# Performance work log

Hardware: AMD Instinct MI355X
Metric: run time of the kernel (lower is better)

Reference implementation:

```python
import jax, jax.numpy as jnp
import numpy as np

NUM_HEADS = 16
HEAD_DIM = 64
Q_DIM = K_DIM = V_DIM = 1024
LQ = LK = 4096
TAU = HEAD_DIM ** (-0.5)


def setup_inputs() -> dict:
    key = jax.random.key(0)
    ks = jax.random.split(key, 11)
    inner = NUM_HEADS * HEAD_DIM
    s = 0.02
    return {
        "q": jax.random.normal(ks[0], (LQ, Q_DIM), dtype=jnp.float32),
        "k": jax.random.normal(ks[1], (LK, K_DIM), dtype=jnp.float32),
        "v": jax.random.normal(ks[2], (LK, V_DIM), dtype=jnp.float32),
        "Wq": jax.random.normal(ks[3], (Q_DIM, inner), dtype=jnp.float32) * s,
        "bq": jax.random.normal(ks[4], (inner,), dtype=jnp.float32) * s,
        "Wk": jax.random.normal(ks[5], (K_DIM, inner), dtype=jnp.float32) * s,
        "bk": jax.random.normal(ks[6], (inner,), dtype=jnp.float32) * s,
        "Wv": jax.random.normal(ks[7], (V_DIM, inner), dtype=jnp.float32) * s,
        "bv": jax.random.normal(ks[8], (inner,), dtype=jnp.float32) * s,
        "Wo": jax.random.normal(ks[9], (inner, Q_DIM), dtype=jnp.float32) * s,
        "bo": jax.random.normal(ks[10], (Q_DIM,), dtype=jnp.float32) * s,
    }


def reference(q, k, v, Wq, bq, Wk, bk, Wv, bv, Wo, bo):
    h, x = NUM_HEADS, HEAD_DIM
    # projections: [L, h*x] -> per-head layout
    qh = (q @ Wq + bq).reshape(-1, h, x)  # [Lq, h, x]
    kh = (k @ Wk + bk).reshape(-1, h, x)  # [Lk, h, x]
    vh = (v @ Wv + bv).reshape(-1, h, x)  # [Lk, h, x]
    # scores: [h, Lq, Lk]
    att = jnp.einsum('qhx,khx->hqk', qh, kh) * TAU
    att = jax.nn.softmax(att, axis=-1)  # dropout=0.0 -> identity
    ctx = jnp.einsum('hqk,khx->qhx', att, vh).reshape(-1, h * x)  # [Lq, h*x]
    out = ctx @ Wo + bo  # [Lq, Q_DIM]
    return out, att
```

## Files before the change

kernel.cpp:

```cpp
#include <hip/hip_runtime.h>
#include <hip/hip_bf16.h>

typedef unsigned short ushort_t;
typedef __attribute__((ext_vector_type(8))) short short8;
typedef __attribute__((ext_vector_type(8))) __bf16 bf16x8;
typedef __attribute__((ext_vector_type(4))) float f32x4;

#define LQS 4096
#define LKS 4096
#define NH 16
#define HD 64
#define DIN 1024
static constexpr float TAU_S = 0.125f;

__device__ __forceinline__ ushort_t f32_to_bf16(float x) {
  union { float f; unsigned u; } v; v.f = x;
  unsigned r = v.u + 0x7FFF + ((v.u >> 16) & 1);
  return (ushort_t)(r >> 16);
}

__device__ __forceinline__ void gld_lds16(const void* g, void* l) {
  __builtin_amdgcn_global_load_lds((const __attribute__((address_space(1))) void*)g,
                                   (__attribute__((address_space(3))) void*)l, 16, 0, 0);
}

__device__ __forceinline__ f32x4 mfma16(bf16x8 a, bf16x8 b, f32x4 c) {
  return __builtin_amdgcn_mfma_f32_16x16x32_bf16(a, b, c, 0, 0, 0);
}

__global__ void cvt_kernel(const float* __restrict__ src, ushort_t* __restrict__ dst, int n) {
  int i = (blockIdx.x * 256 + threadIdx.x) * 8;
  if (i + 8 > n) return;
  float4 a = *(const float4*)(src + i);
  float4 b = *(const float4*)(src + i + 4);
  short8 o;
  o[0] = (short)f32_to_bf16(a.x); o[1] = (short)f32_to_bf16(a.y);
  o[2] = (short)f32_to_bf16(a.z); o[3] = (short)f32_to_bf16(a.w);
  o[4] = (short)f32_to_bf16(b.x); o[5] = (short)f32_to_bf16(b.y);
  o[6] = (short)f32_to_bf16(b.z); o[7] = (short)f32_to_bf16(b.w);
  *(short8*)(dst + i) = o;
}

__global__ void transpose_w(const float* __restrict__ W, ushort_t* __restrict__ Wt) {
  __shared__ float tile[64][65];
  const int t = threadIdx.x;
  const int k0 = blockIdx.y * 64, n0 = blockIdx.x * 64;
#pragma unroll
  for (int i = 0; i < 16; ++i) {
    int idx = i * 256 + t;
    int r = idx >> 6, c = idx & 63;
    tile[r][c] = W[(size_t)(k0 + r) * DIN + n0 + c];
  }
  __syncthreads();
#pragma unroll
  for (int i = 0; i < 16; ++i) {
    int idx = i * 256 + t;
    int r = idx >> 6, c = idx & 63;
    Wt[(size_t)(n0 + r) * DIN + k0 + c] = f32_to_bf16(tile[c][r]);
  }
}

__global__ void transpose_v(const ushort_t* __restrict__ vh, ushort_t* __restrict__ vt) {
  __shared__ ushort_t tile[64][65];
  const int t = threadIdx.x;
  const int k0 = blockIdx.x * 64, h = blockIdx.y;
#pragma unroll
  for (int i = 0; i < 16; ++i) {
    int idx = i * 256 + t;
    int r = idx >> 6, c = idx & 63;
    tile[r][c] = vh[(size_t)(k0 + r) * DIN + h * HD + c];
  }
  __syncthreads();
#pragma unroll
  for (int i = 0; i < 16; ++i) {
    int idx = i * 256 + t;
    int r = idx >> 6, c = idx & 63;
    vt[((size_t)h * HD + r) * (size_t)LKS + k0 + c] = tile[c][r];
  }
}

template <bool OUT_F32>
__launch_bounds__(256, 2)
__global__ void gemm_nt(const ushort_t* __restrict__ A, const ushort_t* __restrict__ Bt,
                        const float* __restrict__ bias, void* __restrict__ Cout,
                        int M, int N, int K, float scale) {
  __shared__ __align__(16) ushort_t Alds[128 * 64];
  __shared__ __align__(16) ushort_t Blds[128 * 64];
  const int t = threadIdx.x, wave = t >> 6, lane = t & 63;
  const int l15 = lane & 15, lg = lane >> 4;
  const int m0 = blockIdx.y * 128, n0 = blockIdx.x * 128;
  const int wr = wave >> 1, wc = wave & 1;
  f32x4 acc[4][4];
#pragma unroll
  for (int i = 0; i < 4; ++i)
#pragma unroll
    for (int j = 0; j < 4; ++j) acc[i][j] = (f32x4){0.f, 0.f, 0.f, 0.f};

  for (int tk = 0; tk < K / 64; ++tk) {
#pragma unroll
    for (int c = 0; c < 4; ++c) {
      int chunk = wave * 4 + c;
      int row = chunk * 8 + (lane >> 3);
      int ss = (lane & 7) ^ (row & 7);
      gld_lds16(A + (size_t)(m0 + row) * K + tk * 64 + ss * 8, (char*)Alds + chunk * 1024);
      gld_lds16(Bt + (size_t)(n0 + row) * K + tk * 64 + ss * 8, (char*)Blds + chunk * 1024);
    }
    __syncthreads();
#pragma unroll
    for (int kk = 0; kk < 2; ++kk) {
      bf16x8 a[4], b[4];
#pragma unroll
      for (int i = 0; i < 4; ++i) {
        int ra = wr * 64 + i * 16 + l15;
        a[i] = *(const bf16x8*)((const char*)Alds + ra * 128 + ((((kk * 4 + lg) << 4)) ^ ((ra & 7) << 4)));
        int rb = wc * 64 + i * 16 + l15;
        b[i] = *(const bf16x8*)((const char*)Blds + rb * 128 + ((((kk * 4 + lg) << 4)) ^ ((rb & 7) << 4)));
      }
#pragma unroll
      for (int mi = 0; mi < 4; ++mi)
#pragma unroll
        for (int ni = 0; ni < 4; ++ni)
          acc[mi][ni] = mfma16(a[mi], b[ni], acc[mi][ni]);
    }
    __syncthreads();
  }
#pragma unroll
  for (int ni = 0; ni < 4; ++ni) {
    int coln = n0 + wc * 64 + ni * 16 + l15;
    float bv = bias[coln];
#pragma unroll
    for (int mi = 0; mi < 4; ++mi) {
#pragma unroll
      for (int r = 0; r < 4; ++r) {
        int rowm = m0 + wr * 64 + mi * 16 + lg * 4 + r;
        float v = (acc[mi][ni][r] + bv) * scale;
        if (OUT_F32)
          ((float*)Cout)[(size_t)rowm * N + coln] = v;
        else
          ((ushort_t*)Cout)[(size_t)rowm * N + coln] = f32_to_bf16(v);
      }
    }
  }
}

__launch_bounds__(256, 2)
__global__ void attn_kernel(const ushort_t* __restrict__ qh, const ushort_t* __restrict__ kh,
                            const ushort_t* __restrict__ vt, float* __restrict__ att,
                            ushort_t* __restrict__ ctx) {
  __shared__ __align__(16) ushort_t Klds[64 * 64];
  __shared__ __align__(16) ushort_t Vlds[64 * 64];
  __shared__ __align__(16) ushort_t Plds[64 * 64];
  const int t = threadIdx.x, wave = t >> 6, lane = t & 63;
  const int l15 = lane & 15, lg = lane >> 4;
  const int h = blockIdx.y;
  const int q0 = blockIdx.x * 64;

  bf16x8 qa[2];
  {
    int row = q0 + wave * 16 + l15;
    const ushort_t* qp = qh + (size_t)row * DIN + h * HD + lg * 8;
    qa[0] = *(const bf16x8*)(qp);
    qa[1] = *(const bf16x8*)(qp + 32);
  }

  float rs[4] = {0.f, 0.f, 0.f, 0.f};
  for (int tk = 0; tk < LKS / 64; ++tk) {
#pragma unroll
    for (int c = 0; c < 2; ++c) {
      int chunk = wave * 2 + c;
      int row = chunk * 8 + (lane >> 3);
      int ss = (lane & 7) ^ (row & 7);
      gld_lds16(kh + (size_t)(tk * 64 + row) * DIN + h * HD + ss * 8, (char*)Klds + chunk * 1024);
    }
    __syncthreads();
#pragma unroll
    for (int ct = 0; ct < 4; ++ct) {
      f32x4 acc = (f32x4){0.f, 0.f, 0.f, 0.f};
#pragma unroll
      for (int kk = 0; kk < 2; ++kk) {
        int row = ct * 16 + l15;
        bf16x8 kb = *(const bf16x8*)((const char*)Klds + row * 128 + ((((kk * 4 + lg) << 4)) ^ ((row & 7) << 4)));
        acc = mfma16(qa[kk], kb, acc);
      }
#pragma unroll
      for (int r = 0; r < 4; ++r) rs[r] += __expf(acc[r]);
    }
    __syncthreads();
  }
#pragma unroll
  for (int m = 1; m < 16; m <<= 1) {
#pragma unroll
    for (int r = 0; r < 4; ++r) rs[r] += __shfl_xor(rs[r], m, 64);
  }
  float recip[4];
#pragma unroll
  for (int r = 0; r < 4; ++r) recip[r] = 1.0f / rs[r];

  f32x4 cacc[4];
#pragma unroll
  for (int x = 0; x < 4; ++x) cacc[x] = (f32x4){0.f, 0.f, 0.f, 0.f};
  float* atth = att + ((size_t)h << 24);

  for (int tk = 0; tk < LKS / 64; ++tk) {
#pragma unroll
    for (int c = 0; c < 2; ++c) {
      int chunk = wave * 2 + c;
      int row = chunk * 8 + (lane >> 3);
      int ss = (lane & 7) ^ (row & 7);
      gld_lds16(kh + (size_t)(tk * 64 + row) * DIN + h * HD + ss * 8, (char*)Klds + chunk * 1024);
      gld_lds16(vt + ((size_t)h * HD + row) * (size_t)LKS + tk * 64 + ss * 8, (char*)Vlds + chunk * 1024);
    }
    __syncthreads();
#pragma unroll
    for (int ct = 0; ct < 4; ++ct) {
      f32x4 acc = (f32x4){0.f, 0.f, 0.f, 0.f};
#pragma unroll
      for (int kk = 0; kk < 2; ++kk) {
        int row = ct * 16 + l15;
        bf16x8 kb = *(const bf16x8*)((const char*)Klds + row * 128 + ((((kk * 4 + lg) << 4)) ^ ((row & 7) << 4)));
        acc = mfma16(qa[kk], kb, acc);
      }
#pragma unroll
      for (int r = 0; r < 4; ++r) {
        float p = __expf(acc[r]) * recip[r];
        int rowq = q0 + wave * 16 + lg * 4 + r;
        int col = tk * 64 + ct * 16 + l15;
        atth[((size_t)rowq << 12) + col] = p;
        int R = wave * 16 + lg * 4 + r;
        int byte = R * 128 + ((ct * 32 + l15 * 2) ^ ((R & 7) << 4));
        *(ushort_t*)((char*)Plds + byte) = f32_to_bf16(p);
      }
    }
    bf16x8 pa[2];
#pragma unroll
    for (int kk = 0; kk < 2; ++kk) {
      int R = wave * 16 + l15;
      pa[kk] = *(const bf16x8*)((const char*)Plds + R * 128 + ((((kk * 4 + lg) << 4)) ^ ((R & 7) << 4)));
    }
#pragma unroll
    for (int x = 0; x < 4; ++x) {
#pragma unroll
      for (int kk = 0; kk < 2; ++kk) {
        int rv = x * 16 + l15;
        bf16x8 vb = *(const bf16x8*)((const char*)Vlds + rv * 128 + ((((kk * 4 + lg) << 4)) ^ ((rv & 7) << 4)));
        cacc[x] = mfma16(pa[kk], vb, cacc[x]);
      }
    }
    __syncthreads();
  }
#pragma unroll
  for (int x = 0; x < 4; ++x) {
#pragma unroll
    for (int r = 0; r < 4; ++r) {
      int rowq = q0 + wave * 16 + lg * 4 + r;
      int col = h * HD + x * 16 + l15;
      ctx[(size_t)rowq * DIN + col] = f32_to_bf16(cacc[x][r]);
    }
  }
}

extern "C" void kernel_launch(void* const* d_in, const int* in_sizes, int n_in,
                              void* d_out, int out_size, void* d_ws, size_t ws_size,
                              hipStream_t stream) {
  const float* q = (const float*)d_in[0];
  const float* k = (const float*)d_in[1];
  const float* v = (const float*)d_in[2];
  const float* Wq = (const float*)d_in[3];
  const float* bq = (const float*)d_in[4];
  const float* Wk = (const float*)d_in[5];
  const float* bk = (const float*)d_in[6];
  const float* Wv = (const float*)d_in[7];
  const float* bv = (const float*)d_in[8];
  const float* Wo = (const float*)d_in[9];
  const float* bo = (const float*)d_in[10];

  float* out = (float*)d_out;
  float* att = out + (size_t)LQS * DIN;

  char* ws = (char*)d_ws;
  ushort_t* qhb = (ushort_t*)(ws + (size_t)0);
  ushort_t* khb = (ushort_t*)(ws + ((size_t)8 << 20));
  ushort_t* vhb = (ushort_t*)(ws + ((size_t)16 << 20));
  ushort_t* vtb = (ushort_t*)(ws + ((size_t)24 << 20));
  ushort_t* ctx = (ushort_t*)(ws + ((size_t)32 << 20));
  ushort_t* qb = (ushort_t*)(ws + ((size_t)40 << 20));
  ushort_t* kb = (ushort_t*)(ws + ((size_t)48 << 20));
  ushort_t* vb = (ushort_t*)(ws + ((size_t)56 << 20));
  ushort_t* Wqt = (ushort_t*)(ws + ((size_t)64 << 20));
  ushort_t* Wkt = (ushort_t*)(ws + ((size_t)66 << 20));
  ushort_t* Wvt = (ushort_t*)(ws + ((size_t)68 << 20));
  ushort_t* Wot = (ushort_t*)(ws + ((size_t)70 << 20));

  const int n = LQS * DIN;
  cvt_kernel<<<n / 8 / 256, 256, 0, stream>>>(q, qb, n);
  cvt_kernel<<<n / 8 / 256, 256, 0, stream>>>(k, kb, n);
  cvt_kernel<<<n / 8 / 256, 256, 0, stream>>>(v, vb, n);

  dim3 tg(16, 16);
  transpose_w<<<tg, 256, 0, stream>>>(Wq, Wqt);
  transpose_w<<<tg, 256, 0, stream>>>(Wk, Wkt);
  transpose_w<<<tg, 256, 0, stream>>>(Wv, Wvt);
  transpose_w<<<tg, 256, 0, stream>>>(Wo, Wot);

  dim3 gg(DIN / 128, LQS / 128);
  gemm_nt<false><<<gg, 256, 0, stream>>>(qb, Wqt, bq, qhb, LQS, DIN, DIN, TAU_S);
  gemm_nt<false><<<gg, 256, 0, stream>>>(kb, Wkt, bk, khb, LQS, DIN, DIN, 1.0f);
  gemm_nt<false><<<gg, 256, 0, stream>>>(vb, Wvt, bv, vhb, LQS, DIN, DIN, 1.0f);

  transpose_v<<<dim3(64, 16), 256, 0, stream>>>(vhb, vtb);

  attn_kernel<<<dim3(LQS / 64, NH), 256, 0, stream>>>(qhb, khb, vtb, att, ctx);

  gemm_nt<true><<<gg, 256, 0, stream>>>(ctx, Wot, bo, out, LQS, DIN, DIN, 1.0f);
}
```

Before: 472.6 us.

## Double-buffer K/V tiles in attention, batch launches, and use exp2 with folded scale

The attention kernel now runs 512-thread blocks over 128 query rows. K and V tiles are double-buffered in LDS so the next tile's load overlaps the current tile's compute, and each wave keeps a private P buffer. Softmax switches from __expf to hardware exp2, with log2(e) folded into the Q projection scale. The three conversion kernels, four weight transposes and three projection GEMMs are each merged into one batched launch via blockIdx.z, cutting launch count. The larger block and extra LDS may reduce occupancy; the output is still dominated by writing the full fp32 attention matrix.

```diff
diff --git a/kernel.cpp b/kernel.cpp
--- a/kernel.cpp
+++ b/kernel.cpp
@@ -11,7 +11,12 @@
 #define NH 16
 #define HD 64
 #define DIN 1024
+#define QBLK 128
+#define KVB 64
 static constexpr float TAU_S = 0.125f;
+static constexpr float LOG2E = 1.4426950408889634f;
+
+__device__ __forceinline__ float exp2_fast(float x) { return __builtin_amdgcn_exp2f(x); }
 
 __device__ __forceinline__ ushort_t f32_to_bf16(float x) {
   union { float f; unsigned u; } v; v.f = x;
@@ -28,9 +33,11 @@
   return __builtin_amdgcn_mfma_f32_16x16x32_bf16(a, b, c, 0, 0, 0);
 }
 
-__global__ void cvt_kernel(const float* __restrict__ src, ushort_t* __restrict__ dst, int n) {
+struct Cvt3 { const float* src[3]; ushort_t* dst[3]; };
+__global__ void cvt_kernel(Cvt3 c) {
+  const float* __restrict__ src = c.src[blockIdx.y];
+  ushort_t* __restrict__ dst = c.dst[blockIdx.y];
   int i = (blockIdx.x * 256 + threadIdx.x) * 8;
-  if (i + 8 > n) return;
   float4 a = *(const float4*)(src + i);
   float4 b = *(const float4*)(src + i + 4);
   short8 o;
@@ -41,7 +48,10 @@
   *(short8*)(dst + i) = o;
 }
 
-__global__ void transpose_w(const float* __restrict__ W, ushort_t* __restrict__ Wt) {
+struct TW4 { const float* W[4]; ushort_t* Wt[4]; };
+__global__ void transpose_w(TW4 w) {
+  const float* __restrict__ W = w.W[blockIdx.z];
+  ushort_t* __restrict__ Wt = w.Wt[blockIdx.z];
   __shared__ float tile[64][65];
   const int t = threadIdx.x;
   const int k0 = blockIdx.y * 64, n0 = blockIdx.x * 64;
@@ -79,11 +89,24 @@
   }
 }
 
+struct Batch3 {
+  const ushort_t* A[3];
+  const ushort_t* Bt[3];
+  const float* bias[3];
+  void* C[3];
+  float scale[3];
+};
 template <bool OUT_F32>
 __launch_bounds__(256, 2)
-__global__ void gemm_nt(const ushort_t* __restrict__ A, const ushort_t* __restrict__ Bt,
-                        const float* __restrict__ bias, void* __restrict__ Cout,
-                        int M, int N, int K, float scale) {
+__global__ void gemm_nt(Batch3 bt3) {
+  const int z = blockIdx.z;
+  const ushort_t* __restrict__ A = bt3.A[z];
+  const ushort_t* __restrict__ Bt = bt3.Bt[z];
+  const float* __restrict__ bias = bt3.bias[z];
+  void* __restrict__ Cout = bt3.C[z];
+  const float scale = bt3.scale[z];
+  const int K = DIN, N = DIN;
+
   __shared__ __align__(16) ushort_t Alds[128 * 64];
   __shared__ __align__(16) ushort_t Blds[128 * 64];
   const int t = threadIdx.x, wave = t >> 6, lane = t & 63;
@@ -143,17 +166,22 @@
   }
 }
 
-__launch_bounds__(256, 2)
+__launch_bounds__(512, 4)
 __global__ void attn_kernel(const ushort_t* __restrict__ qh, const ushort_t* __restrict__ kh,
                             const ushort_t* __restrict__ vt, float* __restrict__ att,
                             ushort_t* __restrict__ ctx) {
-  __shared__ __align__(16) ushort_t Klds[64 * 64];
-  __shared__ __align__(16) ushort_t Vlds[64 * 64];
-  __shared__ __align__(16) ushort_t Plds[64 * 64];
+  __shared__ __align__(16) ushort_t Klds[2][KVB * 64];
+  __shared__ __align__(16) ushort_t Vlds[2][KVB * 64];
+  __shared__ __align__(16) ushort_t Plds[8][16 * KVB];
   const int t = threadIdx.x, wave = t >> 6, lane = t & 63;
   const int l15 = lane & 15, lg = lane >> 4;
   const int h = blockIdx.y;
-  const int q0 = blockIdx.x * 64;
+  const int q0 = blockIdx.x * QBLK;
+
+  const int srow = t >> 3;
+  const int sslot = (t & 7) ^ (srow & 7);
+  const ushort_t* kbase = kh + (size_t)srow * DIN + h * HD + sslot * 8;
+  const ushort_t* vbase = vt + ((size_t)h * HD + srow) * (size_t)LKS + sslot * 8;
 
   bf16x8 qa[2];
   {
@@ -164,28 +192,26 @@
   }
 
   float rs[4] = {0.f, 0.f, 0.f, 0.f};
-  for (int tk = 0; tk < LKS / 64; ++tk) {
-#pragma unroll
-    for (int c = 0; c < 2; ++c) {
-      int chunk = wave * 2 + c;
-      int row = chunk * 8 + (lane >> 3);
-      int ss = (lane & 7) ^ (row & 7);
-      gld_lds16(kh + (size_t)(tk * 64 + row) * DIN + h * HD + ss * 8, (char*)Klds + chunk * 1024);
-    }
-    __syncthreads();
+  gld_lds16(kbase, (char*)Klds[0] + wave * 1024);
+  __syncthreads();
+  int cur = 0;
+  for (int tk = 0; tk < LKS / KVB; ++tk) {
+    if (tk + 1 < LKS / KVB)
+      gld_lds16(kbase + (size_t)(tk + 1) * KVB * DIN, (char*)Klds[cur ^ 1] + wave * 1024);
 #pragma unroll
     for (int ct = 0; ct < 4; ++ct) {
       f32x4 acc = (f32x4){0.f, 0.f, 0.f, 0.f};
 #pragma unroll
       for (int kk = 0; kk < 2; ++kk) {
         int row = ct * 16 + l15;
-        bf16x8 kb = *(const bf16x8*)((const char*)Klds + row * 128 + ((((kk * 4 + lg) << 4)) ^ ((row & 7) << 4)));
+        bf16x8 kb = *(const bf16x8*)((const char*)Klds[cur] + row * 128 + ((((kk * 4 + lg) << 4)) ^ ((row & 7) << 4)));
         acc = mfma16(qa[kk], kb, acc);
       }
 #pragma unroll
-      for (int r = 0; r < 4; ++r) rs[r] += __expf(acc[r]);
+      for (int r = 0; r < 4; ++r) rs[r] += exp2_fast(acc[r]);
     }
     __syncthreads();
+    cur ^= 1;
   }
 #pragma unroll
   for (int m = 1; m < 16; m <<= 1) {
@@ -201,52 +227,52 @@
   for (int x = 0; x < 4; ++x) cacc[x] = (f32x4){0.f, 0.f, 0.f, 0.f};
   float* atth = att + ((size_t)h << 24);
 
-  for (int tk = 0; tk < LKS / 64; ++tk) {
-#pragma unroll
-    for (int c = 0; c < 2; ++c) {
-      int chunk = wave * 2 + c;
-      int row = chunk * 8 + (lane >> 3);
-      int ss = (lane & 7) ^ (row & 7);
-      gld_lds16(kh + (size_t)(tk * 64 + row) * DIN + h * HD + ss * 8, (char*)Klds + chunk * 1024);
-      gld_lds16(vt + ((size_t)h * HD + row) * (size_t)LKS + tk * 64 + ss * 8, (char*)Vlds + chunk * 1024);
-    }
-    __syncthreads();
+  gld_lds16(kbase, (char*)Klds[0] + wave * 1024);
+  gld_lds16(vbase, (char*)Vlds[0] + wave * 1024);
+  __syncthreads();
+  cur = 0;
+  for (int tk = 0; tk < LKS / KVB; ++tk) {
+    if (tk + 1 < LKS / KVB) {
+      gld_lds16(kbase + (size_t)(tk + 1) * KVB * DIN, (char*)Klds[cur ^ 1] + wave * 1024);
+      gld_lds16(vbase + (tk + 1) * KVB, (char*)Vlds[cur ^ 1] + wave * 1024);
+    }
 #pragma unroll
     for (int ct = 0; ct < 4; ++ct) {
       f32x4 acc = (f32x4){0.f, 0.f, 0.f, 0.f};
 #pragma unroll
       for (int kk = 0; kk < 2; ++kk) {
         int row = ct * 16 + l15;
-        bf16x8 kb = *(const bf16x8*)((const char*)Klds + row * 128 + ((((kk * 4 + lg) << 4)) ^ ((row & 7) << 4)));
+        bf16x8 kb = *(const bf16x8*)((const char*)Klds[cur] + row * 128 + ((((kk * 4 + lg) << 4)) ^ ((row & 7) << 4)));
         acc = mfma16(qa[kk], kb, acc);
       }
 #pragma unroll
       for (int r = 0; r < 4; ++r) {
-        float p = __expf(acc[r]) * recip[r];
+        float p = exp2_fast(acc[r]) * recip[r];
         int rowq = q0 + wave * 16 + lg * 4 + r;
-        int col = tk * 64 + ct * 16 + l15;
+        int col = tk * KVB + ct * 16 + l15;
         atth[((size_t)rowq << 12) + col] = p;
-        int R = wave * 16 + lg * 4 + r;
+        int R = lg * 4 + r;
         int byte = R * 128 + ((ct * 32 + l15 * 2) ^ ((R & 7) << 4));
-        *(ushort_t*)((char*)Plds + byte) = f32_to_bf16(p);
+        *(ushort_t*)((char*)Plds[wave] + byte) = f32_to_bf16(p);
       }
     }
     bf16x8 pa[2];
 #pragma unroll
     for (int kk = 0; kk < 2; ++kk) {
-      int R = wave * 16 + l15;
-      pa[kk] = *(const bf16x8*)((const char*)Plds + R * 128 + ((((kk * 4 + lg) << 4)) ^ ((R & 7) << 4)));
+      int R = l15;
+      pa[kk] = *(const bf16x8*)((const char*)Plds[wave] + R * 128 + ((((kk * 4 + lg) << 4)) ^ ((R & 7) << 4)));
     }
 #pragma unroll
     for (int x = 0; x < 4; ++x) {
 #pragma unroll
       for (int kk = 0; kk < 2; ++kk) {
         int rv = x * 16 + l15;
-        bf16x8 vb = *(const bf16x8*)((const char*)Vlds + rv * 128 + ((((kk * 4 + lg) << 4)) ^ ((rv & 7) << 4)));
+        bf16x8 vb = *(const bf16x8*)((const char*)Vlds[cur] + rv * 128 + ((((kk * 4 + lg) << 4)) ^ ((rv & 7) << 4)));
         cacc[x] = mfma16(pa[kk], vb, cacc[x]);
       }
     }
     __syncthreads();
+    cur ^= 1;
   }
 #pragma unroll
   for (int x = 0; x < 4; ++x) {
@@ -291,25 +317,33 @@
   ushort_t* Wvt = (ushort_t*)(ws + ((size_t)68 << 20));
   ushort_t* Wot = (ushort_t*)(ws + ((size_t)70 << 20));
 
-  const int n = LQS * DIN;
-  cvt_kernel<<<n / 8 / 256, 256, 0, stream>>>(q, qb, n);
-  cvt_kernel<<<n / 8 / 256, 256, 0, stream>>>(k, kb, n);
-  cvt_kernel<<<n / 8 / 256, 256, 0, stream>>>(v, vb, n);
-
-  dim3 tg(16, 16);
-  transpose_w<<<tg, 256, 0, stream>>>(Wq, Wqt);
-  transpose_w<<<tg, 256, 0, stream>>>(Wk, Wkt);
-  transpose_w<<<tg, 256, 0, stream>>>(Wv, Wvt);
-  transpose_w<<<tg, 256, 0, stream>>>(Wo, Wot);
-
-  dim3 gg(DIN / 128, LQS / 128);
-  gemm_nt<false><<<gg, 256, 0, stream>>>(qb, Wqt, bq, qhb, LQS, DIN, DIN, TAU_S);
-  gemm_nt<false><<<gg, 256, 0, stream>>>(kb, Wkt, bk, khb, LQS, DIN, DIN, 1.0f);
-  gemm_nt<false><<<gg, 256, 0, stream>>>(vb, Wvt, bv, vhb, LQS, DIN, DIN, 1.0f);
+  Cvt3 c3;
+  c3.src[0] = q; c3.src[1] = k; c3.src[2] = v;
+  c3.dst[0] = qb; c3.dst[1] = kb; c3.dst[2] = vb;
+  cvt_kernel<<<dim3(LQS * DIN / 8 / 256, 3), 256, 0, stream>>>(c3);
+
+  TW4 w4;
+  w4.W[0] = Wq; w4.W[1] = Wk; w4.W[2] = Wv; w4.W[3] = Wo;
+  w4.Wt[0] = Wqt; w4.Wt[1] = Wkt; w4.Wt[2] = Wvt; w4.Wt[3] = Wot;
+  transpose_w<<<dim3(16, 16, 4), 256, 0, stream>>>(w4);
+
+  Batch3 pb;
+  pb.A[0] = qb; pb.A[1] = kb; pb.A[2] = vb;
+  pb.Bt[0] = Wqt; pb.Bt[1] = Wkt; pb.Bt[2] = Wvt;
+  pb.bias[0] = bq; pb.bias[1] = bk; pb.bias[2] = bv;
+  pb.C[0] = qhb; pb.C[1] = khb; pb.C[2] = vhb;
+  pb.scale[0] = TAU_S * LOG2E; pb.scale[1] = 1.0f; pb.scale[2] = 1.0f;
+  gemm_nt<false><<<dim3(DIN / 128, LQS / 128, 3), 256, 0, stream>>>(pb);
 
   transpose_v<<<dim3(64, 16), 256, 0, stream>>>(vhb, vtb);
 
-  attn_kernel<<<dim3(LQS / 64, NH), 256, 0, stream>>>(qhb, khb, vtb, att, ctx);
-
-  gemm_nt<true><<<gg, 256, 0, stream>>>(ctx, Wot, bo, out, LQS, DIN, DIN, 1.0f);
-}
+  attn_kernel<<<dim3(LQS / QBLK, NH), 512, 0, stream>>>(qhb, khb, vtb, att, ctx);
+
+  Batch3 ob;
+  ob.A[0] = ctx; ob.A[1] = ctx; ob.A[2] = ctx;
+  ob.Bt[0] = Wot; ob.Bt[1] = Wot; ob.Bt[2] = Wot;
+  ob.bias[0] = bo; ob.bias[1] = bo; ob.bias[2] = bo;
+  ob.C[0] = out; ob.C[1] = out; ob.C[2] = out;
+  ob.scale[0] = 1.0f; ob.scale[1] = 1.0f; ob.scale[2] = 1.0f;
+  gemm_nt<true><<<dim3(DIN / 128, LQS / 128, 1), 256, 0, stream>>>(ob);
+}
```

After: 490.1 us. +3.7%, slower.
